# Performance work log

Measured on AMD Instinct MI355X. Metric: run time of the kernel, lower is better.

## Reference

```python
import jax, jax.numpy as jnp
import numpy as np

N, T = 8192, 1024
CD = 4            # coord dim = 2*d
H, KD, VD = 2, 8, 8
DA = 8            # att_coeff feature dim
AOD = 16          # attention output dim
LAT, OUT = 64, 32


def setup_inputs() -> dict:
    key = jax.random.key(0)
    ks = jax.random.split(key, 16)
    inp = {
        "coord1": jax.random.normal(ks[0], (N, CD), jnp.float32),
        "coord2": jax.random.normal(ks[1], (N, CD), jnp.float32),
        "att_coeff": jax.random.uniform(ks[2], (T, DA), jnp.float32),
        "local_coords": jax.random.normal(ks[3], (N, T, CD), jnp.float32),
        "mask": jax.random.bernoulli(ks[4], 0.5, (N, 1, T)),
    }
    s = 0.1
    inp["wq"] = jax.random.normal(ks[5], (CD, H * KD), jnp.float32) * s
    inp["bq"] = jnp.zeros((H * KD,), jnp.float32)
    inp["wk"] = jax.random.normal(ks[6], (CD, H * KD), jnp.float32) * s
    inp["bk"] = jnp.zeros((H * KD,), jnp.float32)
    inp["wv"] = jax.random.normal(ks[7], (DA, H * VD), jnp.float32) * s
    inp["bv"] = jnp.zeros((H * VD,), jnp.float32)
    inp["wo"] = jax.random.normal(ks[8], (H * VD, AOD), jnp.float32) * s
    inp["bo"] = jnp.zeros((AOD,), jnp.float32)
    inp["w1"] = jax.random.normal(ks[9], (2 * CD + AOD, LAT), jnp.float32) * s
    inp["b1"] = jnp.zeros((LAT,), jnp.float32)
    inp["w2"] = jax.random.normal(ks[10], (LAT, LAT), jnp.float32) * s
    inp["b2"] = jnp.zeros((LAT,), jnp.float32)
    inp["wout"] = jax.random.normal(ks[11], (LAT, OUT), jnp.float32) * s
    inp["bout"] = jnp.zeros((OUT,), jnp.float32)
    return inp


def reference(coord1, coord2, att_coeff, local_coords, mask,
              wq, bq, wk, bk, wv, bv, wo, bo,
              w1, b1, w2, b2, wout, bout):
    # --- masked attention over gathered neighbor coords ---
    q = (coord1 @ wq + bq).reshape(N, H, KD)              # [N,h,kd]
    k = (local_coords @ wk + bk).reshape(N, T, H, KD)     # [N,T,h,kd]
    v = (att_coeff @ wv + bv).reshape(T, H, VD)           # [T,h,vd]
    logits = jnp.einsum('nhd,nThd->nhT', q, k) / jnp.sqrt(
        jnp.asarray(KD, coord1.dtype))                    # [N,h,T]
    logits = jnp.where(mask, logits, -1e30)
    attw = jax.nn.softmax(logits, axis=-1)
    attn = jnp.einsum('nhT,Thd->nhd', attw, v).reshape(N, H * VD)
    att = jnp.exp(-(attn @ wo + bo))                      # [N,AOD]
    # --- small tanh MLP stack ---
    act = jnp.concatenate([coord1, coord2, att], axis=-1) # [N,2*CD+AOD]
    act = jnp.tanh(act @ w1 + b1)
    act = jnp.tanh(act @ w2 + b2)
    return jnp.tanh(act @ wout + bout)                    # [N,OUT]
```

## Files before the change

### kernel.cpp

```cpp
#include <hip/hip_runtime.h>
#include <cstdint>


__device__ __forceinline__ float bflo(uint32_t u) { return __uint_as_float(u << 16); }
__device__ __forceinline__ float bfhi(uint32_t u) { return __uint_as_float(u & 0xFFFF0000u); }
__device__ __forceinline__ uint32_t f2bf(float f) {
    uint32_t x = __float_as_uint(f);
    return (x + 0x7FFFu + ((x >> 16) & 1u)) >> 16;
}
__device__ __forceinline__ float ftanh(float x) {
    float e = __expf(2.0f * x);
    return 1.0f - 2.0f / (e + 1.0f);
}

__global__ __launch_bounds__(512)
void attn_phase1(const float* __restrict__ coord1,
                 const float* __restrict__ att_coeff,
                 const float* __restrict__ local_coords,
                 const void*  __restrict__ maskp,
                 const float* __restrict__ Wq, const float* __restrict__ Bq,
                 const float* __restrict__ Wk, const float* __restrict__ Bk,
                 const float* __restrict__ Wv, const float* __restrict__ Bv,
                 float* __restrict__ ws)
{
    __shared__ uint4    vq[2048];
    __shared__ uint32_t mrow[8][256];

    const int tid  = threadIdx.x;
    const int lane = tid & 63;
    const int wid  = tid >> 6;

    uint4 mm = ((const uint4*)maskp)[tid];
    bool ok = (mm.x <= 1u || mm.x == 0x3F800000u) &&
              (mm.y <= 1u || mm.y == 0x3F800000u) &&
              (mm.z <= 1u || mm.z == 0x3F800000u) &&
              (mm.w <= 1u || mm.w == 0x3F800000u);
    const bool m4 = (__all(ok) != 0);

    #pragma unroll
    for (int tt = 0; tt < 2; ++tt) {
        const int t = tid * 2 + tt;
        const float4 a0 = *(const float4*)(att_coeff + t * 8);
        const float4 a1 = *(const float4*)(att_coeff + t * 8 + 4);
        float vr[16];
        #pragma unroll
        for (int o = 0; o < 16; ++o) {
            vr[o] = Bv[o]
                + a0.x * Wv[o]      + a0.y * Wv[16 + o] + a0.z * Wv[32 + o] + a0.w * Wv[48 + o]
                + a1.x * Wv[64 + o] + a1.y * Wv[80 + o] + a1.z * Wv[96 + o] + a1.w * Wv[112 + o];
        }
        #pragma unroll
        for (int h = 0; h < 2; ++h) {
            const int g  = 2 * t + h;
            const int gs = (g & ~7) | ((g ^ (g >> 3)) & 7);
            uint4 pk;
            pk.x = f2bf(vr[h * 8 + 0]) | (f2bf(vr[h * 8 + 1]) << 16);
            pk.y = f2bf(vr[h * 8 + 2]) | (f2bf(vr[h * 8 + 3]) << 16);
            pk.z = f2bf(vr[h * 8 + 4]) | (f2bf(vr[h * 8 + 5]) << 16);
            pk.w = f2bf(vr[h * 8 + 6]) | (f2bf(vr[h * 8 + 7]) << 16);
            vq[gs] = pk;
        }
    }

    const int n = (blockIdx.x << 3) + wid;

    if (m4) {
        const uint4* wp = (const uint4*)((const uint32_t*)maskp + (size_t)n * 1024) + lane * 4;
        uint4 pk;
        uint32_t b[4];
        #pragma unroll
        for (int j = 0; j < 4; ++j) {
            const uint4 w = wp[j];
            b[j] = (w.x ? 1u : 0u) | ((w.y ? 1u : 0u) << 8) |
                   ((w.z ? 1u : 0u) << 16) | ((w.w ? 1u : 0u) << 24);
        }
        pk.x = b[0]; pk.y = b[1]; pk.z = b[2]; pk.w = b[3];
        *(uint4*)&mrow[wid][lane * 4] = pk;
    } else {
        const uint4 w = ((const uint4*)((const uint8_t*)maskp + (size_t)n * 1024))[lane];
        *(uint4*)&mrow[wid][lane * 4] = w;
    }
    __syncthreads();

    const int g0 = 2 * lane;
    const int bg = (g0 & ~7) | ((g0 ^ (g0 >> 3)) & 7);
    const float rs8 = 0.35355339059327373f;

    float A[2][4], Bs[2];
    {
        const float4 c1 = *(const float4*)(coord1 + n * 4);
        float q[16];
        #pragma unroll
        for (int o = 0; o < 16; ++o)
            q[o] = Bq[o] + c1.x * Wq[o] + c1.y * Wq[16 + o] + c1.z * Wq[32 + o] + c1.w * Wq[48 + o];
        #pragma unroll
        for (int h = 0; h < 2; ++h) {
            #pragma unroll
            for (int c = 0; c < 4; ++c) {
                float s = 0.f;
                #pragma unroll
                for (int d = 0; d < 8; ++d) s += q[h * 8 + d] * Wk[c * 16 + h * 8 + d];
                A[h][c] = s * rs8;
            }
            float s2 = 0.f;
            #pragma unroll
            for (int d = 0; d < 8; ++d) s2 += q[h * 8 + d] * Bk[h * 8 + d];
            Bs[h] = s2 * rs8;
        }
    }

    const float4* lcp = (const float4*)local_coords + (size_t)n * 1024 + lane;
    const int  mword = lane >> 2;
    const int  msh   = (lane & 3) * 8;

    float p[16];
    #pragma unroll
    for (int k = 0; k < 16; ++k) p[k] = 0.f;
    float s0 = 0.f, s1 = 0.f;

    #pragma unroll 4
    for (int i = 0; i < 16; ++i) {
        const float4 lc = lcp[i * 64];
        const uint32_t mw = mrow[wid][mword + 16 * i];
        const bool keep = ((mw >> msh) & 0xFFu) != 0u;
        const float v0 = Bs[0] + lc.x * A[0][0] + lc.y * A[0][1] + lc.z * A[0][2] + lc.w * A[0][3];
        const float v1 = Bs[1] + lc.x * A[1][0] + lc.y * A[1][1] + lc.z * A[1][2] + lc.w * A[1][3];
        const float e0 = keep ? __expf(v0) : 0.f;
        const float e1 = keep ? __expf(v1) : 0.f;
        s0 += e0; s1 += e1;
        const uint4 w0 = vq[(bg + (i << 7))];
        const uint4 w1 = vq[(bg + (i << 7)) ^ 1];
        p[0]  += e0 * bflo(w0.x); p[1]  += e0 * bfhi(w0.x);
        p[2]  += e0 * bflo(w0.y); p[3]  += e0 * bfhi(w0.y);
        p[4]  += e0 * bflo(w0.z); p[5]  += e0 * bfhi(w0.z);
        p[6]  += e0 * bflo(w0.w); p[7]  += e0 * bfhi(w0.w);
        p[8]  += e1 * bflo(w1.x); p[9]  += e1 * bfhi(w1.x);
        p[10] += e1 * bflo(w1.y); p[11] += e1 * bfhi(w1.y);
        p[12] += e1 * bflo(w1.z); p[13] += e1 * bfhi(w1.z);
        p[14] += e1 * bflo(w1.w); p[15] += e1 * bfhi(w1.w);
    }

    #pragma unroll
    for (int s = 32; s; s >>= 1) {
        s0 += __shfl_xor(s0, s, 64);
        s1 += __shfl_xor(s1, s, 64);
    }

    if (s0 == 0.0f) {
        #pragma unroll 2
        for (int i = 0; i < 16; ++i) {
            const uint4 w0 = vq[(bg + (i << 7))];
            const uint4 w1 = vq[(bg + (i << 7)) ^ 1];
            p[0]  += bflo(w0.x); p[1]  += bfhi(w0.x);
            p[2]  += bflo(w0.y); p[3]  += bfhi(w0.y);
            p[4]  += bflo(w0.z); p[5]  += bfhi(w0.z);
            p[6]  += bflo(w0.w); p[7]  += bfhi(w0.w);
            p[8]  += bflo(w1.x); p[9]  += bfhi(w1.x);
            p[10] += bflo(w1.y); p[11] += bfhi(w1.y);
            p[12] += bflo(w1.z); p[13] += bfhi(w1.z);
            p[14] += bflo(w1.w); p[15] += bfhi(w1.w);
        }
        s0 = 1024.0f; s1 = 1024.0f;
    }

    {
        const bool h5 = (lane & 32) != 0;
        #pragma unroll
        for (int k = 0; k < 8; ++k) {
            const float snd = h5 ? p[k] : p[k + 8];
            const float kp  = h5 ? p[k + 8] : p[k];
            p[k] = kp + __shfl_xor(snd, 32, 64);
        }
        const bool h4 = (lane & 16) != 0;
        #pragma unroll
        for (int k = 0; k < 4; ++k) {
            const float snd = h4 ? p[k] : p[k + 4];
            const float kp  = h4 ? p[k + 4] : p[k];
            p[k] = kp + __shfl_xor(snd, 16, 64);
        }
        const bool h3 = (lane & 8) != 0;
        #pragma unroll
        for (int k = 0; k < 2; ++k) {
            const float snd = h3 ? p[k] : p[k + 2];
            const float kp  = h3 ? p[k + 2] : p[k];
            p[k] = kp + __shfl_xor(snd, 8, 64);
        }
        const bool h2 = (lane & 4) != 0;
        {
            const float snd = h2 ? p[0] : p[1];
            const float kp  = h2 ? p[1] : p[0];
            p[0] = kp + __shfl_xor(snd, 4, 64);
        }
        p[0] += __shfl_xor(p[0], 2, 64);
        p[0] += __shfl_xor(p[0], 1, 64);
    }

    if ((lane & 3) == 0)
        ws[(size_t)n * 16 + (lane >> 2)] = p[0] / (lane >= 32 ? s1 : s0);
}

__global__ void attn_phase2(const float* __restrict__ coord1,
                            const float* __restrict__ coord2,
                            const float* __restrict__ ws,
                            const float* __restrict__ Wo, const float* __restrict__ Bo,
                            const float* __restrict__ W1, const float* __restrict__ B1,
                            const float* __restrict__ W2, const float* __restrict__ B2,
                            const float* __restrict__ Wt, const float* __restrict__ Bt,
                            float* __restrict__ out)
{
    const int lane = threadIdx.x & 63;
    const int wid  = threadIdx.x >> 6;
    const int n    = (blockIdx.x << 2) + wid;

    const float4 c1 = *(const float4*)(coord1 + n * 4);
    const float4 c2 = *(const float4*)(coord2 + n * 4);
    const float  av = ws[(size_t)n * 16 + (lane & 15)];

    float attv;
    {
        const int j = lane & 15;
        float acc = Bo[j];
        #pragma unroll
        for (int c = 0; c < 16; ++c)
            acc += __shfl(av, c, 64) * Wo[c * 16 + j];
        attv = __expf(-acc);
    }

    float a1;
    {
        float acc = B1[lane];
        acc += c1.x * W1[0 * 64 + lane] + c1.y * W1[1 * 64 + lane]
             + c1.z * W1[2 * 64 + lane] + c1.w * W1[3 * 64 + lane];
        acc += c2.x * W1[4 * 64 + lane] + c2.y * W1[5 * 64 + lane]
             + c2.z * W1[6 * 64 + lane] + c2.w * W1[7 * 64 + lane];
        #pragma unroll
        for (int c = 0; c < 16; ++c)
            acc += __shfl(attv, c, 64) * W1[(8 + c) * 64 + lane];
        a1 = ftanh(acc);
    }

    float a2;
    {
        float acc = B2[lane];
        #pragma unroll
        for (int c = 0; c < 64; ++c)
            acc += __shfl(a1, c, 64) * W2[c * 64 + lane];
        a2 = ftanh(acc);
    }

    {
        const int j = lane & 31;
        float acc = Bt[j];
        #pragma unroll
        for (int c = 0; c < 64; ++c)
            acc += __shfl(a2, c, 64) * Wt[c * 32 + j];
        if (lane < 32) out[(size_t)n * 32 + lane] = ftanh(acc);
    }
}

extern "C" void kernel_launch(void* const* d_in, const int* in_sizes, int n_in,
                              void* d_out, int out_size, void* d_ws, size_t ws_size,
                              hipStream_t stream) {
    (void)in_sizes; (void)n_in; (void)out_size; (void)ws_size;
    float* ws = (float*)d_ws;
    attn_phase1<<<1024, 512, 0, stream>>>(
        (const float*)d_in[0],  (const float*)d_in[2],
        (const float*)d_in[3],  d_in[4],
        (const float*)d_in[5],  (const float*)d_in[6],
        (const float*)d_in[7],  (const float*)d_in[8],
        (const float*)d_in[9],  (const float*)d_in[10],
        ws);
    attn_phase2<<<2048, 256, 0, stream>>>(
        (const float*)d_in[0],  (const float*)d_in[1],
        ws,
        (const float*)d_in[11], (const float*)d_in[12],
        (const float*)d_in[13], (const float*)d_in[14],
        (const float*)d_in[15], (const float*)d_in[16],
        (const float*)d_in[17], (const float*)d_in[18],
        (float*)d_out);
}
```

Baseline: 58.41 us.

## Stream local_coords through a per-wave LDS ring with async global_load_lds

Replaces the direct global float4 loads of local_coords with a 4-deep per-wave ring buffer in LDS, filled via global_load_lds and gated by explicit vmcnt/lgkmcnt waits. The intent is to keep several global loads in flight ahead of the exp/accumulate work and hide memory latency on this bandwidth-bound stream. It adds 32KB of LDS per block, which may cut occupancy, and uses hand-placed waitcnts and sched barriers that constrain the compiler's scheduling.

```diff
diff --git a/kernel.cpp b/kernel.cpp
--- a/kernel.cpp
+++ b/kernel.cpp
@@ -25,6 +25,7 @@
 {
     __shared__ uint4    vq[2048];
     __shared__ uint32_t mrow[8][256];
+    __shared__ float4   ring[8][4][64];
 
     const int tid  = threadIdx.x;
     const int lane = tid & 63;
@@ -118,27 +119,58 @@
     for (int k = 0; k < 16; ++k) p[k] = 0.f;
     float s0 = 0.f, s1 = 0.f;
 
-    #pragma unroll 4
-    for (int i = 0; i < 16; ++i) {
-        const float4 lc = lcp[i * 64];
-        const uint32_t mw = mrow[wid][mword + 16 * i];
-        const bool keep = ((mw >> msh) & 0xFFu) != 0u;
-        const float v0 = Bs[0] + lc.x * A[0][0] + lc.y * A[0][1] + lc.z * A[0][2] + lc.w * A[0][3];
-        const float v1 = Bs[1] + lc.x * A[1][0] + lc.y * A[1][1] + lc.z * A[1][2] + lc.w * A[1][3];
-        const float e0 = keep ? __expf(v0) : 0.f;
-        const float e1 = keep ? __expf(v1) : 0.f;
-        s0 += e0; s1 += e1;
-        const uint4 w0 = vq[(bg + (i << 7))];
-        const uint4 w1 = vq[(bg + (i << 7)) ^ 1];
-        p[0]  += e0 * bflo(w0.x); p[1]  += e0 * bfhi(w0.x);
-        p[2]  += e0 * bflo(w0.y); p[3]  += e0 * bfhi(w0.y);
-        p[4]  += e0 * bflo(w0.z); p[5]  += e0 * bfhi(w0.z);
-        p[6]  += e0 * bflo(w0.w); p[7]  += e0 * bfhi(w0.w);
-        p[8]  += e1 * bflo(w1.x); p[9]  += e1 * bfhi(w1.x);
-        p[10] += e1 * bflo(w1.y); p[11] += e1 * bfhi(w1.y);
-        p[12] += e1 * bflo(w1.z); p[13] += e1 * bfhi(w1.z);
-        p[14] += e1 * bflo(w1.w); p[15] += e1 * bfhi(w1.w);
-    }
+    #pragma unroll
+    for (int s = 0; s < 4; ++s)
+        __builtin_amdgcn_global_load_lds((const uint32_t*)(lcp + s * 64),
+                                         (uint32_t*)&ring[wid][s][0], 16, 0, 0);
+
+#define COMPUTE(LC, I)                                                        \
+    {                                                                         \
+        const uint32_t mw = mrow[wid][mword + 16 * (I)];                      \
+        const bool keep = ((mw >> msh) & 0xFFu) != 0u;                        \
+        const float v0 = Bs[0] + (LC).x * A[0][0] + (LC).y * A[0][1]          \
+                               + (LC).z * A[0][2] + (LC).w * A[0][3];         \
+        const float v1 = Bs[1] + (LC).x * A[1][0] + (LC).y * A[1][1]          \
+                               + (LC).z * A[1][2] + (LC).w * A[1][3];         \
+        const float e0 = keep ? __expf(v0) : 0.f;                             \
+        const float e1 = keep ? __expf(v1) : 0.f;                             \
+        s0 += e0; s1 += e1;                                                   \
+        const uint4 w0 = vq[(bg + ((I) << 7))];                               \
+        const uint4 w1 = vq[(bg + ((I) << 7)) ^ 1];                           \
+        p[0]  += e0 * bflo(w0.x); p[1]  += e0 * bfhi(w0.x);                   \
+        p[2]  += e0 * bflo(w0.y); p[3]  += e0 * bfhi(w0.y);                   \
+        p[4]  += e0 * bflo(w0.z); p[5]  += e0 * bfhi(w0.z);                   \
+        p[6]  += e0 * bflo(w0.w); p[7]  += e0 * bfhi(w0.w);                   \
+        p[8]  += e1 * bflo(w1.x); p[9]  += e1 * bfhi(w1.x);                   \
+        p[10] += e1 * bflo(w1.y); p[11] += e1 * bfhi(w1.y);                   \
+        p[12] += e1 * bflo(w1.z); p[13] += e1 * bfhi(w1.z);                   \
+        p[14] += e1 * bflo(w1.w); p[15] += e1 * bfhi(w1.w);                   \
+    }
+
+    #pragma unroll 1
+    for (int i = 0; i < 12; ++i) {
+        asm volatile("s_waitcnt vmcnt(3)" ::: "memory");
+        __builtin_amdgcn_sched_barrier(0);
+        const float4 lc4 = ring[wid][i & 3][lane];
+        asm volatile("s_waitcnt lgkmcnt(0)" ::: "memory");
+        __builtin_amdgcn_sched_barrier(0);
+        __builtin_amdgcn_global_load_lds((const uint32_t*)(lcp + (i + 4) * 64),
+                                         (uint32_t*)&ring[wid][i & 3][0], 16, 0, 0);
+        COMPUTE(lc4, i);
+    }
+    asm volatile("s_waitcnt vmcnt(0)" ::: "memory");
+    __builtin_amdgcn_sched_barrier(0);
+    {
+        const float4 lcA = ring[wid][0][lane];
+        const float4 lcB = ring[wid][1][lane];
+        const float4 lcC = ring[wid][2][lane];
+        const float4 lcD = ring[wid][3][lane];
+        COMPUTE(lcA, 12);
+        COMPUTE(lcB, 13);
+        COMPUTE(lcC, 14);
+        COMPUTE(lcD, 15);
+    }
+#undef COMPUTE
 
     #pragma unroll
     for (int s = 32; s; s >>= 1) {
```

New measurement: 56.93 us. 2.5% less time.
